# Kernel tuning notes

Measured on AMD Instinct MI355X. Metric: run time of the kernel, lower is better.

The kernel has to match this reference:

```python
import jax, jax.numpy as jnp
import numpy as np

NUM_USERS = 100000
NUM_ITEMS = 100000
EMBED_DIM = 64
BATCH = 16384
MAX_DEG = 50


def setup_inputs() -> dict:
    key = jax.random.key(0)
    ks = jax.random.split(key, 16)
    inp = {
        'nodes_u': jax.random.randint(ks[0], (BATCH,), 0, NUM_USERS),
        'nodes_v': jax.random.randint(ks[1], (BATCH,), 0, NUM_ITEMS),
        'u_neibs': jax.random.randint(ks[2], (BATCH, MAX_DEG), 0, NUM_USERS),
        'v_neibs': jax.random.randint(ks[3], (BATCH, MAX_DEG), 0, NUM_ITEMS),
        'u_mask': jax.random.randint(ks[4], (BATCH, MAX_DEG), 0, 2).astype(bool),
        'v_mask': jax.random.randint(ks[5], (BATCH, MAX_DEG), 0, 2).astype(bool),
        'u_sel': jax.random.uniform(ks[6], (BATCH, MAX_DEG), dtype=jnp.float32),
        'v_sel': jax.random.uniform(ks[7], (BATCH, MAX_DEG), dtype=jnp.float32),
        # learned parameters
        'u2e': jax.random.normal(ks[8], (NUM_USERS, EMBED_DIM), dtype=jnp.float32) * 0.1,
        'v2e': jax.random.normal(ks[9], (NUM_ITEMS, EMBED_DIM), dtype=jnp.float32) * 0.1,
        'Wu': jax.random.normal(ks[10], (2 * EMBED_DIM, EMBED_DIM), dtype=jnp.float32) * 0.05,
        'bu': jnp.zeros((EMBED_DIM,), dtype=jnp.float32),
        'Wv': jax.random.normal(ks[11], (2 * EMBED_DIM, EMBED_DIM), dtype=jnp.float32) * 0.05,
        'bv': jnp.zeros((EMBED_DIM,), dtype=jnp.float32),
    }
    return inp


def _side_embed(nodes, neibs, mask, sel, table, W, b):
    # nodes: [B] int, neibs: [B,K] int, mask: [B,K] bool, sel: [B,K] float
    self_emb = table[nodes]                                  # [B, D]
    w = sel * mask.astype(sel.dtype)                         # [B, K]
    nemb = table[neibs] * w[..., None]                       # [B, K, D]
    cnt = mask.astype(sel.dtype).sum(-1)                     # [B] true degree
    agg = nemb.sum(1) / jnp.maximum(cnt, 1.0)[:, None]       # sel-weighted mean over neighbors
    lin = jnp.concatenate([self_emb, agg], axis=-1) @ W + b  # [B, D]
    # deg == 0 -> raw self embedding (matches torch branch)
    return jnp.where((cnt > 0)[:, None], lin, self_emb)


def reference(nodes_u, nodes_v, u_neibs, v_neibs, u_mask, v_mask,
              u_sel, v_sel, u2e, v2e, Wu, bu, Wv, bv):
    Uembs = _side_embed(nodes_u, u_neibs, u_mask, u_sel, u2e, Wu, bu)
    Vembs = _side_embed(nodes_v, v_neibs, v_mask, v_sel, v2e, Wv, bv)
    return (Uembs * Vembs).sum(-1)  # [B]
```

## Files before the change

### kernel.cpp

```cpp
#include <hip/hip_runtime.h>


constexpr int KDEG  = 50;
constexpr int DIM   = 64;
constexpr int SLOTS = 56;
constexpr int EPB   = 16;

template <typename MT>
__device__ __forceinline__ void load_meta(const void* __restrict__ mask_p,
                                          const float* __restrict__ sel,
                                          const int* __restrict__ neibs,
                                          int base, int lane,
                                          int& idx, float& w, bool& act) {
  if (lane < KDEG) {
    MT m    = ((const MT*)mask_p)[base + lane];
    float s = sel[base + lane];
    idx     = neibs[base + lane];
    act     = (m != (MT)0);
    w       = act ? s : 0.0f;
  } else { idx = 0; w = 0.0f; act = false; }
}

__device__ __forceinline__ int compact_side(int lane, int idx, float w, bool act,
                                            int2* __restrict__ spair) {
  unsigned long long balA = __ballot(act);
  unsigned long long balI = __ballot(!act && (lane < SLOTS));
  int cnt = __popcll(balA);
  unsigned long long below = (1ULL << lane) - 1ULL;
  int pos = act ? __popcll(balA & below)
                : cnt + __popcll(balI & below);
  if (lane < SLOTS) {
    spair[pos] = make_int2(act ? idx : 0, act ? __float_as_int(w) : 0);
  }
  return cnt;
}

__global__ __launch_bounds__(512, 8) void fused_graphsage_dot(
    const int* __restrict__ nodes_u, const int* __restrict__ nodes_v,
    const int* __restrict__ u_neibs, const int* __restrict__ v_neibs,
    const void* __restrict__ u_mask_p, const void* __restrict__ v_mask_p,
    const float* __restrict__ u_sel, const float* __restrict__ v_sel,
    const float* __restrict__ u2e, const float* __restrict__ v2e,
    const float* __restrict__ Wu, const float* __restrict__ bu,
    const float* __restrict__ Wv, const float* __restrict__ bv,
    float* __restrict__ out)
{
  __shared__ float sx  [EPB][256];
  __shared__ float slin[2][EPB][DIM];
  __shared__ int2  spair[EPB][2][SLOTS];
  __shared__ int   slay;

  const int lane = threadIdx.x & 63;
  const int wvid = threadIdx.x >> 6;
  const int eb0  = blockIdx.x * EPB;
  const int e0   = wvid * 2, e1 = e0 + 1;
  const int g0   = eb0 + e0, g1 = eb0 + e1;
  const int b0   = g0 * KDEG, b1 = g1 * KDEG;

  float self_u0 = u2e[(size_t)nodes_u[g0] * DIM + lane];
  float self_v0 = v2e[(size_t)nodes_v[g0] * DIM + lane];
  float self_u1 = u2e[(size_t)nodes_u[g1] * DIM + lane];
  float self_v1 = v2e[(size_t)nodes_v[g1] * DIM + lane];

  if (wvid == 0) {
    uchar4 b4 = ((const uchar4*)u_mask_p)[lane];
    bool gt1  = (b4.x > 1) | (b4.y > 1) | (b4.z > 1) | (b4.w > 1);
    bool offw = ((b4.y | b4.z | b4.w) != 0);
    unsigned long long bg = __ballot(gt1);
    unsigned long long bo = __ballot(offw);
    if (lane == 0) slay = bg ? 2 : (bo ? 1 : 0);
  }
  __syncthreads();
  const int lay = slay;

  int iu0, iv0, iu1, iv1; float wu0, wv0, wu1, wv1; bool au0_, av0_, au1_, av1_;
  if (lay == 0) {
    load_meta<int>(u_mask_p, u_sel, u_neibs, b0, lane, iu0, wu0, au0_);
    load_meta<int>(v_mask_p, v_sel, v_neibs, b0, lane, iv0, wv0, av0_);
    load_meta<int>(u_mask_p, u_sel, u_neibs, b1, lane, iu1, wu1, au1_);
    load_meta<int>(v_mask_p, v_sel, v_neibs, b1, lane, iv1, wv1, av1_);
  } else if (lay == 1) {
    load_meta<unsigned char>(u_mask_p, u_sel, u_neibs, b0, lane, iu0, wu0, au0_);
    load_meta<unsigned char>(v_mask_p, v_sel, v_neibs, b0, lane, iv0, wv0, av0_);
    load_meta<unsigned char>(u_mask_p, u_sel, u_neibs, b1, lane, iu1, wu1, au1_);
    load_meta<unsigned char>(v_mask_p, v_sel, v_neibs, b1, lane, iv1, wv1, av1_);
  } else {
    load_meta<float>(u_mask_p, u_sel, u_neibs, b0, lane, iu0, wu0, au0_);
    load_meta<float>(v_mask_p, v_sel, v_neibs, b0, lane, iv0, wv0, av0_);
    load_meta<float>(u_mask_p, u_sel, u_neibs, b1, lane, iu1, wu1, au1_);
    load_meta<float>(v_mask_p, v_sel, v_neibs, b1, lane, iv1, wv1, av1_);
  }
  const int cnt_u0 = compact_side(lane, iu0, wu0, au0_, spair[e0][0]);
  const int cnt_v0 = compact_side(lane, iv0, wv0, av0_, spair[e0][1]);
  const int cnt_u1 = compact_side(lane, iu1, wu1, au1_, spair[e1][0]);
  const int cnt_v1 = compact_side(lane, iv1, wv1, av1_, spair[e1][1]);

  float accu0 = 0.f, accv0 = 0.f, accu1 = 0.f, accv1 = 0.f;
  {
    const int2* __restrict__ pU0 = spair[e0][0];
    const int2* __restrict__ pV0 = spair[e0][1];
    const int2* __restrict__ pU1 = spair[e1][0];
    const int2* __restrict__ pV1 = spair[e1][1];
    int cmax = max(max(cnt_u0, cnt_v0), max(cnt_u1, cnt_v1));
    int cm4  = (cmax + 3) & ~3;
    for (int s = 0; s < cm4; s += 4) {
      #pragma unroll
      for (int j = 0; j < 4; ++j) {
        const int t = s + j;
        int2 a = pU0[t];
        int2 b = pV0[t];
        int2 c = pU1[t];
        int2 d = pV1[t];
        accu0 = fmaf(__int_as_float(a.y), u2e[(size_t)a.x * DIM + lane], accu0);
        accv0 = fmaf(__int_as_float(b.y), v2e[(size_t)b.x * DIM + lane], accv0);
        accu1 = fmaf(__int_as_float(c.y), u2e[(size_t)c.x * DIM + lane], accu1);
        accv1 = fmaf(__int_as_float(d.y), v2e[(size_t)d.x * DIM + lane], accv1);
      }
    }
  }

  sx[e0][lane]       = self_u0;
  sx[e0][ 64 + lane] = accu0 * (1.0f / fmaxf((float)cnt_u0, 1.0f));
  sx[e0][128 + lane] = self_v0;
  sx[e0][192 + lane] = accv0 * (1.0f / fmaxf((float)cnt_v0, 1.0f));
  sx[e1][lane]       = self_u1;
  sx[e1][ 64 + lane] = accu1 * (1.0f / fmaxf((float)cnt_u1, 1.0f));
  sx[e1][128 + lane] = self_v1;
  sx[e1][192 + lane] = accv1 * (1.0f / fmaxf((float)cnt_v1, 1.0f));
  __syncthreads();

  {
    const int side = wvid & 1;
    const int eb   = (wvid >> 1) * 4;
    const float* __restrict__ W = side ? Wv : Wu;
    const float  bias = side ? bv[lane] : bu[lane];
    float a0 = bias, a1 = bias, a2 = bias, a3 = bias;
    const int xoff = side * 128;

    #pragma unroll 2
    for (int k4 = 0; k4 < 32; ++k4) {
      const int k = k4 * 4;
      float w0 = W[(k + 0) * DIM + lane];
      float w1 = W[(k + 1) * DIM + lane];
      float w2 = W[(k + 2) * DIM + lane];
      float w3 = W[(k + 3) * DIM + lane];
      float4 x0 = *(const float4*)&sx[eb + 0][xoff + k];
      float4 x1 = *(const float4*)&sx[eb + 1][xoff + k];
      float4 x2 = *(const float4*)&sx[eb + 2][xoff + k];
      float4 x3 = *(const float4*)&sx[eb + 3][xoff + k];
      a0 = fmaf(x0.x, w0, a0); a0 = fmaf(x0.y, w1, a0);
      a0 = fmaf(x0.z, w2, a0); a0 = fmaf(x0.w, w3, a0);
      a1 = fmaf(x1.x, w0, a1); a1 = fmaf(x1.y, w1, a1);
      a1 = fmaf(x1.z, w2, a1); a1 = fmaf(x1.w, w3, a1);
      a2 = fmaf(x2.x, w0, a2); a2 = fmaf(x2.y, w1, a2);
      a2 = fmaf(x2.z, w2, a2); a2 = fmaf(x2.w, w3, a2);
      a3 = fmaf(x3.x, w0, a3); a3 = fmaf(x3.y, w1, a3);
      a3 = fmaf(x3.z, w2, a3); a3 = fmaf(x3.w, w3, a3);
    }
    slin[side][eb + 0][lane] = a0;
    slin[side][eb + 1][lane] = a1;
    slin[side][eb + 2][lane] = a2;
    slin[side][eb + 3][lane] = a3;
  }
  __syncthreads();

  {
    float ue = (cnt_u0 > 0) ? slin[0][e0][lane] : sx[e0][lane];
    float ve = (cnt_v0 > 0) ? slin[1][e0][lane] : sx[e0][128 + lane];
    float p = ue * ve;
    #pragma unroll
    for (int off = 32; off > 0; off >>= 1) p += __shfl_xor(p, off, 64);
    if (lane == 0) out[g0] = p;
  }
  {
    float ue = (cnt_u1 > 0) ? slin[0][e1][lane] : sx[e1][lane];
    float ve = (cnt_v1 > 0) ? slin[1][e1][lane] : sx[e1][128 + lane];
    float p = ue * ve;
    #pragma unroll
    for (int off = 32; off > 0; off >>= 1) p += __shfl_xor(p, off, 64);
    if (lane == 0) out[g1] = p;
  }
}

extern "C" void kernel_launch(void* const* d_in, const int* in_sizes, int n_in,
                              void* d_out, int out_size, void* d_ws, size_t ws_size,
                              hipStream_t stream) {
  const int*   nodes_u = (const int*)  d_in[0];
  const int*   nodes_v = (const int*)  d_in[1];
  const int*   u_neibs = (const int*)  d_in[2];
  const int*   v_neibs = (const int*)  d_in[3];
  const void*  u_mask  =               d_in[4];
  const void*  v_mask  =               d_in[5];
  const float* u_sel   = (const float*)d_in[6];
  const float* v_sel   = (const float*)d_in[7];
  const float* u2e     = (const float*)d_in[8];
  const float* v2e     = (const float*)d_in[9];
  const float* Wu      = (const float*)d_in[10];
  const float* bu      = (const float*)d_in[11];
  const float* Wv      = (const float*)d_in[12];
  const float* bv      = (const float*)d_in[13];
  float* out = (float*)d_out;

  const int batch = in_sizes[0];
  fused_graphsage_dot<<<batch / EPB, 512, 0, stream>>>(
      nodes_u, nodes_v, u_neibs, v_neibs, u_mask, v_mask, u_sel, v_sel,
      u2e, v2e, Wu, bu, Wv, bv, out);
}
```

Measured before the change: 53.87 us.

## Software-pipeline neighbor gathers with double-buffered register banks and split idx/weight arrays

The compacted neighbor list moves from interleaved int2 pairs to separate shared index and weight arrays. The aggregation loop is restructured into a two-bank register prefetch: embedding rows for the next 4 slots per side are issued while FMAs consume the previous bank, keeping about 32 gathers in flight. The goal is to hide global-memory gather latency. The cost is 32 extra live registers under a launch bound of 512 threads and 8 blocks, which leaves a very tight VGPR budget and risks spills. At least 8 slots are now always processed.

```diff
diff --git a/kernel.cpp b/kernel.cpp
--- a/kernel.cpp
+++ b/kernel.cpp
@@ -22,7 +22,8 @@
 }
 
 __device__ __forceinline__ int compact_side(int lane, int idx, float w, bool act,
-                                            int2* __restrict__ spair) {
+                                            int* __restrict__ sidx,
+                                            float* __restrict__ sw) {
   unsigned long long balA = __ballot(act);
   unsigned long long balI = __ballot(!act && (lane < SLOTS));
   int cnt = __popcll(balA);
@@ -30,7 +31,8 @@
   int pos = act ? __popcll(balA & below)
                 : cnt + __popcll(balI & below);
   if (lane < SLOTS) {
-    spair[pos] = make_int2(act ? idx : 0, act ? __float_as_int(w) : 0);
+    sidx[pos] = act ? idx : 0;
+    sw[pos]   = act ? w   : 0.0f;
   }
   return cnt;
 }
@@ -47,7 +49,8 @@
 {
   __shared__ float sx  [EPB][256];
   __shared__ float slin[2][EPB][DIM];
-  __shared__ int2  spair[EPB][2][SLOTS];
+  __shared__ int   sidx[EPB][2][SLOTS];
+  __shared__ float swt [EPB][2][SLOTS];
   __shared__ int   slay;
 
   const int lane = threadIdx.x & 63;
@@ -90,33 +93,55 @@
     load_meta<float>(u_mask_p, u_sel, u_neibs, b1, lane, iu1, wu1, au1_);
     load_meta<float>(v_mask_p, v_sel, v_neibs, b1, lane, iv1, wv1, av1_);
   }
-  const int cnt_u0 = compact_side(lane, iu0, wu0, au0_, spair[e0][0]);
-  const int cnt_v0 = compact_side(lane, iv0, wv0, av0_, spair[e0][1]);
-  const int cnt_u1 = compact_side(lane, iu1, wu1, au1_, spair[e1][0]);
-  const int cnt_v1 = compact_side(lane, iv1, wv1, av1_, spair[e1][1]);
+  const int cnt_u0 = compact_side(lane, iu0, wu0, au0_, sidx[e0][0], swt[e0][0]);
+  const int cnt_v0 = compact_side(lane, iv0, wv0, av0_, sidx[e0][1], swt[e0][1]);
+  const int cnt_u1 = compact_side(lane, iu1, wu1, au1_, sidx[e1][0], swt[e1][0]);
+  const int cnt_v1 = compact_side(lane, iv1, wv1, av1_, sidx[e1][1], swt[e1][1]);
 
   float accu0 = 0.f, accv0 = 0.f, accu1 = 0.f, accv1 = 0.f;
   {
-    const int2* __restrict__ pU0 = spair[e0][0];
-    const int2* __restrict__ pV0 = spair[e0][1];
-    const int2* __restrict__ pU1 = spair[e1][0];
-    const int2* __restrict__ pV1 = spair[e1][1];
+    const int*   __restrict__ pI0 = sidx[e0][0];
+    const float* __restrict__ pW0 = swt [e0][0];
+    const int*   __restrict__ pI1 = sidx[e0][1];
+    const float* __restrict__ pW1 = swt [e0][1];
+    const int*   __restrict__ pI2 = sidx[e1][0];
+    const float* __restrict__ pW2 = swt [e1][0];
+    const int*   __restrict__ pI3 = sidx[e1][1];
+    const float* __restrict__ pW3 = swt [e1][1];
+
+    float r0[8], r1[8], r2[8], r3[8];
+
+#define ISSUE_BANK(S, B) do { _Pragma("unroll")                              \
+    for (int j = 0; j < 4; ++j) {                                            \
+      r0[(B)*4 + j] = u2e[(size_t)pI0[(S) + j] * DIM + lane];                \
+      r1[(B)*4 + j] = v2e[(size_t)pI1[(S) + j] * DIM + lane];                \
+      r2[(B)*4 + j] = u2e[(size_t)pI2[(S) + j] * DIM + lane];                \
+      r3[(B)*4 + j] = v2e[(size_t)pI3[(S) + j] * DIM + lane];                \
+    } } while (0)
+
+#define FMA_BANK(S, B) do { _Pragma("unroll")                                \
+    for (int j = 0; j < 4; ++j) {                                            \
+      accu0 = fmaf(pW0[(S) + j], r0[(B)*4 + j], accu0);                      \
+      accv0 = fmaf(pW1[(S) + j], r1[(B)*4 + j], accv0);                      \
+      accu1 = fmaf(pW2[(S) + j], r2[(B)*4 + j], accu1);                      \
+      accv1 = fmaf(pW3[(S) + j], r3[(B)*4 + j], accv1);                      \
+    } } while (0)
+
     int cmax = max(max(cnt_u0, cnt_v0), max(cnt_u1, cnt_v1));
-    int cm4  = (cmax + 3) & ~3;
-    for (int s = 0; s < cm4; s += 4) {
-      #pragma unroll
-      for (int j = 0; j < 4; ++j) {
-        const int t = s + j;
-        int2 a = pU0[t];
-        int2 b = pV0[t];
-        int2 c = pU1[t];
-        int2 d = pV1[t];
-        accu0 = fmaf(__int_as_float(a.y), u2e[(size_t)a.x * DIM + lane], accu0);
-        accv0 = fmaf(__int_as_float(b.y), v2e[(size_t)b.x * DIM + lane], accv0);
-        accu1 = fmaf(__int_as_float(c.y), u2e[(size_t)c.x * DIM + lane], accu1);
-        accv1 = fmaf(__int_as_float(d.y), v2e[(size_t)d.x * DIM + lane], accv1);
-      }
+    int cm8  = (cmax + 7) & ~7;
+    if (cm8 < 8) cm8 = 8;
+
+    ISSUE_BANK(0, 0);
+    ISSUE_BANK(4, 1);
+    int s = 0;
+    for (; s + 8 < cm8; s += 8) {
+      FMA_BANK(s, 0);     ISSUE_BANK(s + 8, 0);
+      FMA_BANK(s + 4, 1); ISSUE_BANK(s + 12, 1);
     }
+    FMA_BANK(s, 0);
+    FMA_BANK(s + 4, 1);
+#undef ISSUE_BANK
+#undef FMA_BANK
   }
 
   sx[e0][lane]       = self_u0;
```

After: 98.63 us. +83.1%, slower.
